# Optimization experiments

Hardware: AMD Instinct MI355X
Metric: run time of the kernel (lower is better)

Reference implementation:

```python
import jax, jax.numpy as jnp
import numpy as np

EPS = 1e-5

def _bn_relu(y, mean, var, scale, bias):
    # y: (b, c, n); eval-mode batchnorm over channel axis, then ReLU
    inv = scale / jnp.sqrt(var + EPS)
    return jax.nn.relu((y - mean[None, :, None]) * inv[None, :, None] + bias[None, :, None])

def setup_inputs() -> dict:
    key = jax.random.key(0)
    ks = jax.random.split(key, 6)
    b, c, n, cr = 4, 256, 4096, 32
    inp = {
        'x': jax.random.normal(ks[0], (b, c, n), jnp.float32),
        'w_q': jax.random.normal(ks[1], (cr, c), jnp.float32) * (1.0 / np.sqrt(c)),
        'w_k': jax.random.normal(ks[2], (cr, c), jnp.float32) * (1.0 / np.sqrt(c)),
        'w_v': jax.random.normal(ks[3], (c, c), jnp.float32) * (1.0 / np.sqrt(c)),
        'bn1_scale': jnp.ones((cr,), jnp.float32), 'bn1_bias': jnp.zeros((cr,), jnp.float32),
        'bn1_mean': jnp.zeros((cr,), jnp.float32), 'bn1_var': jnp.ones((cr,), jnp.float32),
        'bn2_scale': jnp.ones((cr,), jnp.float32), 'bn2_bias': jnp.zeros((cr,), jnp.float32),
        'bn2_mean': jnp.zeros((cr,), jnp.float32), 'bn2_var': jnp.ones((cr,), jnp.float32),
        'bn3_scale': jnp.ones((c,), jnp.float32), 'bn3_bias': jnp.zeros((c,), jnp.float32),
        'bn3_mean': jnp.zeros((c,), jnp.float32), 'bn3_var': jnp.ones((c,), jnp.float32),
        'gamma': jax.random.normal(ks[4], (1,), jnp.float32),
    }
    return inp

def reference(x, w_q, w_k, w_v,
              bn1_scale, bn1_bias, bn1_mean, bn1_var,
              bn2_scale, bn2_bias, bn2_mean, bn2_var,
              bn3_scale, bn3_bias, bn3_mean, bn3_var,
              gamma):
    # x: (b, c, n). Original views as (b, c, n, 1) so width=1, height=n.
    b, c, n = x.shape
    # 1x1 conv == channel matmul, then BN+ReLU
    q = _bn_relu(jnp.einsum('oc,bcn->bon', w_q, x), bn1_mean, bn1_var, bn1_scale, bn1_bias)  # (b, c', n)
    k = _bn_relu(jnp.einsum('oc,bcn->bon', w_k, x), bn2_mean, bn2_var, bn2_scale, bn2_bias)  # (b, c', n)
    v = _bn_relu(jnp.einsum('oc,bcn->bon', w_v, x), bn3_mean, bn3_var, bn3_scale, bn3_bias)  # (b, c, n)
    # energy_H: (b, n, n) with -inf diagonal (self-attention along 'height')
    energy_h = jnp.einsum('bdi,bdj->bij', q, k)
    eye = jnp.eye(n, dtype=bool)
    energy_h = jnp.where(eye[None], -jnp.inf, energy_h)
    # energy_W: width=1 -> per-position self energy (b, n)
    energy_w = jnp.sum(q * k, axis=1)
    # softmax over concat of n H-logits and 1 W-logit
    att = jax.nn.softmax(jnp.concatenate([energy_h, energy_w[..., None]], axis=-1), axis=-1)  # (b, n, n+1)
    att_h = att[..., :n]        # (b, n, n), query i -> key j
    att_w = att[..., n]         # (b, n)
    out_h = jnp.einsum('bcj,bij->bci', v, att_h)   # aggregate values along height
    out_w = v * att_w[:, None, :]                  # width=1 self term
    out = gamma[0] * (out_h + out_w) + x
    return out
```

## Files before the change

kernel.cpp:

```cpp
#include <hip/hip_runtime.h>

#define Bb 4
#define Cc 256
#define Nn 4096
#define CR 32
#define EPS_BN 1e-5f
#define SHIFT2 28.853900817779268f
#define LOG2E  1.4426950408889634f
#define JSPLIT 2
#define JSL (Nn / JSPLIT)
#define TJ 128
#define NTILES (JSL / TJ)

typedef __attribute__((ext_vector_type(8))) short short8;
typedef __attribute__((ext_vector_type(4))) float f32x4;

__device__ inline unsigned int pk2(float a, float b) {
    __bf16 ha = (__bf16)a, hb = (__bf16)b;
    unsigned short ra = __builtin_bit_cast(unsigned short, ha);
    unsigned short rb = __builtin_bit_cast(unsigned short, hb);
    return ((unsigned int)rb << 16) | ra;
}
__device__ inline float blo(unsigned int u) { return __uint_as_float(u << 16); }
__device__ inline float bhi(unsigned int u) { return __uint_as_float(u & 0xffff0000u); }
__device__ inline float ex2(float x) { return __builtin_amdgcn_exp2f(x); }

__global__ __launch_bounds__(256) void prep_w(
    const float* __restrict__ wq, const float* __restrict__ wk,
    const float* __restrict__ wv, __bf16* __restrict__ Wf)
{
    const int r16 = blockIdx.x;
    const int tid = threadIdx.x;
#pragma unroll
    for (int ss = 0; ss < 2; ++ss) {
        int s = tid + ss * 256;
        int kc = s >> 6, lane = s & 63;
        int R = r16 * 16 + (lane & 15);
        const float* src = (R < 32) ? (wq + (size_t)R * Cc)
                         : (R < 64) ? (wk + (size_t)(R - 32) * Cc)
                                    : (wv + (size_t)(R - 64) * Cc);
        const float* p = src + kc * 32 + (lane >> 4) * 8;
        float4 a = *(const float4*)p;
        float4 c2 = *(const float4*)(p + 4);
        uint4 pk = { pk2(a.x,a.y), pk2(a.z,a.w), pk2(c2.x,c2.y), pk2(c2.z,c2.w) };
        *(uint4*)&Wf[(((size_t)r16 * 8 + kc) * 64 + lane) * 8] = pk;
    }
}

__global__ __launch_bounds__(256) void split_x(
    const float* __restrict__ x,
    __bf16* __restrict__ xhi, __bf16* __restrict__ xlo)
{
    __shared__ __align__(16) float tile[64][68];
    const int tid = threadIdx.x;
    const int n0 = blockIdx.x * 64, c0 = blockIdx.y * 64, b = blockIdx.z;

    {
        int r = tid >> 2, q = tid & 3;
        const float* src = &x[(size_t)(b * Cc + c0 + r) * Nn + n0 + q * 16];
#pragma unroll
        for (int u = 0; u < 4; ++u)
            *(float4*)&tile[r][q * 16 + u * 4] = *(const float4*)&src[u * 4];
    }
    __syncthreads();

    {
        int nr = tid >> 2, oc = tid & 3;
        uint4 H[2], L[2];
#pragma unroll
        for (int u = 0; u < 2; ++u) {
            float h[8], lo8[8];
#pragma unroll
            for (int j = 0; j < 8; ++j) {
                float v = tile[oc * 16 + u * 8 + j][nr];
                float hh = (float)(__bf16)v;
                h[j] = hh; lo8[j] = v - hh;
            }
            H[u] = (uint4){ pk2(h[0],h[1]), pk2(h[2],h[3]), pk2(h[4],h[5]), pk2(h[6],h[7]) };
            L[u] = (uint4){ pk2(lo8[0],lo8[1]), pk2(lo8[2],lo8[3]), pk2(lo8[4],lo8[5]), pk2(lo8[6],lo8[7]) };
        }
        size_t base = (size_t)(b * Nn + n0 + nr) * Cc + c0 + oc * 16;
        *(uint4*)&xhi[base]     = H[0];
        *(uint4*)&xhi[base + 8] = H[1];
        *(uint4*)&xlo[base]     = L[0];
        *(uint4*)&xlo[base + 8] = L[1];
    }
}

__global__ __launch_bounds__(256) void qkv_kernel(
    const __bf16* __restrict__ xhi, const __bf16* __restrict__ xlo,
    const __bf16* __restrict__ Wf,
    const float* __restrict__ bn1s, const float* __restrict__ bn1b, const float* __restrict__ bn1m, const float* __restrict__ bn1v,
    const float* __restrict__ bn2s, const float* __restrict__ bn2b, const float* __restrict__ bn2m, const float* __restrict__ bn2v,
    const float* __restrict__ bn3s, const float* __restrict__ bn3b, const float* __restrict__ bn3m, const float* __restrict__ bn3v,
    __bf16* __restrict__ Qt, __bf16* __restrict__ Kt, __bf16* __restrict__ Vb)
{
    __shared__ __align__(16) __bf16 oT[128 * 136];

    const int tid = threadIdx.x;
    const int n0 = blockIdx.x * 128, g = blockIdx.y, b = blockIdx.z;
    const int lane = tid & 63, w = tid >> 6;
    const int l15 = lane & 15, l4 = lane >> 4;
    const int nmt = (g == 0) ? 4 : 8;
    const int r16b = (g == 0) ? 0 : 4 + (g - 1) * 8;

    const size_t bfoff = (size_t)(b * Nn + n0 + w * 32 + l15) * Cc + l4 * 8;
    const __bf16* bh0 = xhi + bfoff;
    const __bf16* bl0 = xlo + bfoff;

    f32x4 acc[8][2];
#pragma unroll
    for (int mt = 0; mt < 8; ++mt)
#pragma unroll
        for (int nt = 0; nt < 2; ++nt) acc[mt][nt] = (f32x4){0.f, 0.f, 0.f, 0.f};

    for (int kc = 0; kc < 8; ++kc) {
        short8 bh[2], bl[2];
#pragma unroll
        for (int nt = 0; nt < 2; ++nt) {
            bh[nt] = *(const short8*)&bh0[(size_t)(nt * 16) * Cc + kc * 32];
            bl[nt] = *(const short8*)&bl0[(size_t)(nt * 16) * Cc + kc * 32];
        }
#pragma unroll
        for (int mt = 0; mt < 8; ++mt) {
            if (mt < nmt) {
                short8 af = *(const short8*)&Wf[(((size_t)(r16b + mt) * 8 + kc) * 64 + lane) * 8];
#pragma unroll
                for (int nt = 0; nt < 2; ++nt) {
                    acc[mt][nt] = __builtin_amdgcn_mfma_f32_16x16x32_bf16(af, bh[nt], acc[mt][nt], 0, 0, 0);
                    acc[mt][nt] = __builtin_amdgcn_mfma_f32_16x16x32_bf16(af, bl[nt], acc[mt][nt], 0, 0, 0);
                }
            }
        }
    }

    if (g == 0) {
#pragma unroll
        for (int mt = 0; mt < 4; ++mt) {
            float scl[4], off[4];
#pragma unroll
            for (int r = 0; r < 4; ++r) {
                int R = mt * 16 + l4 * 4 + r;
                float s, o;
                if (R < 32) {
                    s = bn1s[R] * __frsqrt_rn(bn1v[R] + EPS_BN);
                    o = bn1b[R] - bn1m[R] * s;
                } else {
                    int row = R - 32;
                    s = bn2s[row] * __frsqrt_rn(bn2v[row] + EPS_BN);
                    o = bn2b[row] - bn2m[row] * s;
                    s *= LOG2E; o *= LOG2E;
                }
                scl[r] = s; off[r] = o;
            }
            __bf16* dst = (mt < 2) ? Qt : Kt;
            int d0 = (mt & 1) * 16 + l4 * 4;
#pragma unroll
            for (int nt = 0; nt < 2; ++nt) {
                f32x4 a = acc[mt][nt];
                float e0 = fmaxf(fmaf(a.x, scl[0], off[0]), 0.f);
                float e1 = fmaxf(fmaf(a.y, scl[1], off[1]), 0.f);
                float e2 = fmaxf(fmaf(a.z, scl[2], off[2]), 0.f);
                float e3 = fmaxf(fmaf(a.w, scl[3], off[3]), 0.f);
                uint2 p = { pk2(e0, e1), pk2(e2, e3) };
                int n = n0 + w * 32 + nt * 16 + l15;
                *(uint2*)&dst[(size_t)(b * Nn + n) * CR + d0] = p;
            }
        }
    } else {
        const int vr0 = (g - 1) * 128;
#pragma unroll
        for (int mt = 0; mt < 8; ++mt) {
            float scl[4], off[4];
#pragma unroll
            for (int r = 0; r < 4; ++r) {
                int row = vr0 + mt * 16 + l4 * 4 + r;
                float s = bn3s[row] * __frsqrt_rn(bn3v[row] + EPS_BN);
                scl[r] = s; off[r] = bn3b[row] - bn3m[row] * s;
            }
#pragma unroll
            for (int nt = 0; nt < 2; ++nt) {
                f32x4 a = acc[mt][nt];
                float e[4];
                e[0] = fmaxf(fmaf(a.x, scl[0], off[0]), 0.f);
                e[1] = fmaxf(fmaf(a.y, scl[1], off[1]), 0.f);
                e[2] = fmaxf(fmaf(a.z, scl[2], off[2]), 0.f);
                e[3] = fmaxf(fmaf(a.w, scl[3], off[3]), 0.f);
                int ncol = w * 32 + nt * 16 + l15;
#pragma unroll
                for (int r = 0; r < 4; ++r)
                    oT[(mt * 16 + l4 * 4 + r) * 136 + ncol] = (__bf16)e[r];
            }
        }
        __syncthreads();
        int rr = tid >> 1, qq = tid & 1;
        size_t vrow = (size_t)(b * Cc + vr0 + rr) * Nn + n0 + qq * 64;
#pragma unroll
        for (int e8 = 0; e8 < 8; ++e8)
            *(uint4*)&Vb[vrow + e8 * 8] = *(const uint4*)&oT[rr * 136 + qq * 64 + e8 * 8];
    }
}

__global__ __launch_bounds__(512) void attn_kernel(
    const __bf16* __restrict__ Qt, const __bf16* __restrict__ Kt,
    const __bf16* __restrict__ Vb,
    __bf16* __restrict__ PO, float* __restrict__ PL)
{
    __shared__ __align__(16) __bf16 sQ[64 * 40];
    __shared__ __align__(16) __bf16 sP[64 * 128];
    __shared__ __align__(16) float  sL[8][64];

    const int tid = threadIdx.x, lane = tid & 63, w = tid >> 6;
    const int b = blockIdx.z, js = blockIdx.y, iblk = blockIdx.x;
    const int i0 = iblk * 64;
    const int l15 = lane & 15, l4 = lane >> 4;

    if (tid < 256) {
        int i = tid >> 2, o = tid & 3;
        *(uint4*)&sQ[i * 40 + o * 8] =
            *(const uint4*)&Qt[(size_t)(b * Nn + i0 + i) * CR + o * 8];
    }
    __syncthreads();

    short8 qf[4];
#pragma unroll
    for (int it = 0; it < 4; ++it)
        qf[it] = *(const short8*)&sQ[(it * 16 + l15) * 40 + l4 * 8];

    f32x4 oacc[8];
#pragma unroll
    for (int z = 0; z < 8; ++z) oacc[z] = (f32x4){0.f, 0.f, 0.f, 0.f};
    float lp[4] = {0.f, 0.f, 0.f, 0.f};

    const size_t jb = (size_t)js * JSL;
    short8 kf = *(const short8*)&Kt[(size_t)(b * Nn + jb + 16 * w + l15) * CR + l4 * 8];
    const __bf16* vrow0 = Vb + (size_t)(b * Cc + w * 32 + l15) * Nn;

    char* sPb = (char*)sP;
    const int wcolw = w * 32 + l4 * 8;

    for (int t = 0; t < NTILES; ++t) {
        const size_t j0 = jb + (size_t)t * TJ;

        short8 v0[2], v1[2];
#pragma unroll
        for (int ct = 0; ct < 2; ++ct)
            v0[ct] = *(const short8*)&vrow0[(size_t)(ct * 16) * Nn + j0 + l4 * 8];
#pragma unroll
        for (int ct = 0; ct < 2; ++ct)
            v1[ct] = *(const short8*)&vrow0[(size_t)(ct * 16) * Nn + j0 + 32 + l4 * 8];

#pragma unroll
        for (int it = 0; it < 4; ++it) {
            f32x4 c0 = (f32x4){0.f, 0.f, 0.f, 0.f};
            c0 = __builtin_amdgcn_mfma_f32_16x16x32_bf16(kf, qf[it], c0, 0, 0, 0);
            float e0 = ex2(c0.x - SHIFT2);
            float e1 = ex2(c0.y - SHIFT2);
            float e2 = ex2(c0.z - SHIFT2);
            float e3 = ex2(c0.w - SHIFT2);
            lp[it] += (e0 + e1) + (e2 + e3);
            uint2 p2 = { pk2(e0, e1), pk2(e2, e3) };
            int row = it * 16 + l15;
            *(uint2*)(sPb + row * 256 + (wcolw ^ ((row & 7) << 4))) = p2;
        }
        __syncthreads();

        if (t + 1 < NTILES)
            kf = *(const short8*)&Kt[(size_t)(b * Nn + j0 + TJ + 16 * w + l15) * CR + l4 * 8];

        __builtin_amdgcn_s_setprio(1);
        {
            short8 pf[4];
#pragma unroll
            for (int it = 0; it < 4; ++it) {
                int row = it * 16 + l15;
                pf[it] = *(const short8*)(sPb + row * 256 + ((l4 * 16) ^ ((row & 7) << 4)));
            }
#pragma unroll
            for (int ct = 0; ct < 2; ++ct)
#pragma unroll
                for (int it = 0; it < 4; ++it)
                    oacc[it * 2 + ct] = __builtin_amdgcn_mfma_f32_16x16x32_bf16(
                        pf[it], v0[ct], oacc[it * 2 + ct], 0, 0, 0);
        }
#pragma unroll
        for (int ct = 0; ct < 2; ++ct)
            v0[ct] = *(const short8*)&vrow0[(size_t)(ct * 16) * Nn + j0 + 64 + l4 * 8];
        {
            short8 pf[4];
#pragma unroll
            for (int it = 0; it < 4; ++it) {
                int row = it * 16 + l15;
                pf[it] = *(const short8*)(sPb + row * 256 + ((64 + l4 * 16) ^ ((row & 7) << 4)));
            }
#pragma unroll
            for (int ct = 0; ct < 2; ++ct)
#pragma unroll
                for (int it = 0; it < 4; ++it)
                    oacc[it * 2 + ct] = __builtin_amdgcn_mfma_f32_16x16x32_bf16(
                        pf[it], v1[ct], oacc[it * 2 + ct], 0, 0, 0);
        }
#pragma unroll
        for (int ct = 0; ct < 2; ++ct)
            v1[ct] = *(const short8*)&vrow0[(size_t)(ct * 16) * Nn + j0 + 96 + l4 * 8];
        {
            short8 pf[4];
#pragma unroll
            for (int it = 0; it < 4; ++it) {
                int row = it * 16 + l15;
                pf[it] = *(const short8*)(sPb + row * 256 + ((128 + l4 * 16) ^ ((row & 7) << 4)));
            }
#pragma unroll
            for (int ct = 0; ct < 2; ++ct)
#pragma unroll
                for (int it = 0; it < 4; ++it)
                    oacc[it * 2 + ct] = __builtin_amdgcn_mfma_f32_16x16x32_bf16(
                        pf[it], v0[ct], oacc[it * 2 + ct], 0, 0, 0);
        }
        {
            short8 pf[4];
#pragma unroll
            for (int it = 0; it < 4; ++it) {
                int row = it * 16 + l15;
                pf[it] = *(const short8*)(sPb + row * 256 + ((192 + l4 * 16) ^ ((row & 7) << 4)));
            }
#pragma unroll
            for (int ct = 0; ct < 2; ++ct)
#pragma unroll
                for (int it = 0; it < 4; ++it)
                    oacc[it * 2 + ct] = __builtin_amdgcn_mfma_f32_16x16x32_bf16(
                        pf[it], v1[ct], oacc[it * 2 + ct], 0, 0, 0);
        }
        __builtin_amdgcn_s_setprio(0);
        __syncthreads();
    }

#pragma unroll
    for (int it = 0; it < 4; ++it) {
        float v = lp[it];
        v += __shfl_xor(v, 16);
        v += __shfl_xor(v, 32);
        if (lane < 16) sL[w][it * 16 + lane] = v;
    }
    __syncthreads();
    if (tid < 64) {
        float s = 0.f;
#pragma unroll
        for (int w8 = 0; w8 < 8; ++w8) s += sL[w8][tid];
        PL[(size_t)(js * Bb + b) * Nn + i0 + tid] = s;
    }

    const size_t base = (size_t)((js * Bb + b) * (Nn / 64) + iblk) * 16384;
#pragma unroll
    for (int it = 0; it < 4; ++it)
#pragma unroll
        for (int ct = 0; ct < 2; ++ct) {
            f32x4 a = oacc[it * 2 + ct];
            uint2 p = { pk2(a.x, a.y), pk2(a.z, a.w) };
            int g16 = w * 2 + ct;
            int s = (g16 >> 2) * 16 + it * 4 + (g16 & 3);
            *(uint2*)&PO[base + (size_t)(s * 64 + lane) * 4] = p;
        }
}

__global__ __launch_bounds__(256) void reduce_kernel(
    const __bf16* __restrict__ PO, const float* __restrict__ PL,
    const float* __restrict__ x, const float* __restrict__ gamma,
    float* __restrict__ out)
{
    __shared__ __align__(16) float oT[64 * 68];
    __shared__ float sLinv[64];

    const int tid = threadIdx.x;
    const int iblk = blockIdx.x, wq = blockIdx.y, b = blockIdx.z;
    const int i0 = iblk * 64;
    const int lane = tid & 63, ct = tid >> 6, l15 = lane & 15, l4 = lane >> 4;

    if (tid < 64) {
        float l = 0.f;
#pragma unroll
        for (int js = 0; js < JSPLIT; ++js)
            l += PL[(size_t)(js * Bb + b) * Nn + i0 + tid];
        sLinv[tid] = 1.0f / l;
    }

    float o[4][4];
#pragma unroll
    for (int it = 0; it < 4; ++it) {
        o[it][0] = o[it][1] = o[it][2] = o[it][3] = 0.f;
#pragma unroll
        for (int js = 0; js < JSPLIT; ++js) {
            size_t base = (size_t)((js * Bb + b) * (Nn / 64) + iblk) * 16384;
            uint2 v = *(const uint2*)&PO[base + (size_t)((((wq * 4 + it) * 4 + ct) * 64 + lane)) * 4];
            o[it][0] += blo(v.x); o[it][1] += bhi(v.x);
            o[it][2] += blo(v.y); o[it][3] += bhi(v.y);
        }
    }

    const int cl = ct * 16 + l15;
#pragma unroll
    for (int it = 0; it < 4; ++it) {
        float4 t4 = { o[it][0], o[it][1], o[it][2], o[it][3] };
        *(float4*)&oT[cl * 68 + it * 16 + l4 * 4] = t4;
    }
    __syncthreads();

    const float g = gamma[0];
    const int c_l = tid >> 2, icol = (tid & 3) * 16;
    const int cg = wq * 64 + c_l;
    const size_t gb = (size_t)(b * Cc + cg) * Nn + i0 + icol;
#pragma unroll
    for (int k4 = 0; k4 < 4; ++k4) {
        float4 ov = *(const float4*)&oT[c_l * 68 + icol + k4 * 4];
        float4 li = *(const float4*)&sLinv[icol + k4 * 4];
        float4 xv = *(const float4*)&x[gb + k4 * 4];
        float4 res;
        res.x = fmaf(g, ov.x * li.x, xv.x);
        res.y = fmaf(g, ov.y * li.y, xv.y);
        res.z = fmaf(g, ov.z * li.z, xv.z);
        res.w = fmaf(g, ov.w * li.w, xv.w);
        *(float4*)&out[gb + k4 * 4] = res;
    }
}

extern "C" void kernel_launch(void* const* d_in, const int* in_sizes, int n_in,
                              void* d_out, int out_size, void* d_ws, size_t ws_size,
                              hipStream_t stream)
{
    const float* x    = (const float*)d_in[0];
    const float* wq   = (const float*)d_in[1];
    const float* wk   = (const float*)d_in[2];
    const float* wv   = (const float*)d_in[3];
    const float* bn1s = (const float*)d_in[4];
    const float* bn1b = (const float*)d_in[5];
    const float* bn1m = (const float*)d_in[6];
    const float* bn1v = (const float*)d_in[7];
    const float* bn2s = (const float*)d_in[8];
    const float* bn2b = (const float*)d_in[9];
    const float* bn2m = (const float*)d_in[10];
    const float* bn2v = (const float*)d_in[11];
    const float* bn3s = (const float*)d_in[12];
    const float* bn3b = (const float*)d_in[13];
    const float* bn3m = (const float*)d_in[14];
    const float* bn3v = (const float*)d_in[15];
    const float* gmm  = (const float*)d_in[16];
    float* out = (float*)d_out;

    char* ws = (char*)d_ws;
    __bf16* Qt  = (__bf16*)(ws);
    __bf16* Kt  = (__bf16*)(ws + (1u << 20));
    __bf16* Vb  = (__bf16*)(ws + (2u << 20));
    __bf16* PO  = (__bf16*)(ws + (10u << 20));
    float*  PL  = (float*)(ws + (26u << 20));
    __bf16* Wf  = (__bf16*)(ws + (26u << 20) + 262144);
    __bf16* xhi = (__bf16*)(ws + (27u << 20));
    __bf16* xlo = (__bf16*)(ws + (35u << 20));

    prep_w<<<dim3(20), 256, 0, stream>>>(wq, wk, wv, Wf);

    split_x<<<dim3(Nn / 64, Cc / 64, Bb), 256, 0, stream>>>(x, xhi, xlo);

    qkv_kernel<<<dim3(Nn / 128, 3, Bb), 256, 0, stream>>>(
        xhi, xlo, Wf,
        bn1s, bn1b, bn1m, bn1v,
        bn2s, bn2b, bn2m, bn2v,
        bn3s, bn3b, bn3m, bn3v,
        Qt, Kt, Vb);

    attn_kernel<<<dim3(Nn / 64, JSPLIT, Bb), 512, 0, stream>>>(Qt, Kt, Vb, PO, PL);

    reduce_kernel<<<dim3(Nn / 64, 4, Bb), 256, 0, stream>>>(PO, PL, x, gmm, out);
}
```

Baseline: 203.0 us.

## Halve attention block to 4 waves, each covering 64 channels and 32 keys

The attention kernel now runs with 256 threads (4 waves) instead of 512. Each wave computes two 16-key score tiles per 128-key tile and accumulates 64 value channels (16 accumulators instead of 8). This doubles per-wave work and register reuse of the P fragments, and halves the redundant P loads from LDS across waves. In exchange each wave holds more registers, which may lower occupancy, and the PO output layout is remapped to match.

```diff
diff --git a/kernel.cpp b/kernel.cpp
--- a/kernel.cpp
+++ b/kernel.cpp
@@ -201,21 +201,21 @@
     }
 }
 
-__global__ __launch_bounds__(512) void attn_kernel(
+__global__ __launch_bounds__(256) void attn_kernel(
     const __bf16* __restrict__ Qt, const __bf16* __restrict__ Kt,
     const __bf16* __restrict__ Vb,
     __bf16* __restrict__ PO, float* __restrict__ PL)
 {
     __shared__ __align__(16) __bf16 sQ[64 * 40];
     __shared__ __align__(16) __bf16 sP[64 * 128];
-    __shared__ __align__(16) float  sL[8][64];
+    __shared__ __align__(16) float  sL[4][64];
 
     const int tid = threadIdx.x, lane = tid & 63, w = tid >> 6;
     const int b = blockIdx.z, js = blockIdx.y, iblk = blockIdx.x;
     const int i0 = iblk * 64;
     const int l15 = lane & 15, l4 = lane >> 4;
 
-    if (tid < 256) {
+    {
         int i = tid >> 2, o = tid & 3;
         *(uint4*)&sQ[i * 40 + o * 8] =
             *(const uint4*)&Qt[(size_t)(b * Nn + i0 + i) * CR + o * 8];
@@ -227,46 +227,55 @@
     for (int it = 0; it < 4; ++it)
         qf[it] = *(const short8*)&sQ[(it * 16 + l15) * 40 + l4 * 8];
 
-    f32x4 oacc[8];
-#pragma unroll
-    for (int z = 0; z < 8; ++z) oacc[z] = (f32x4){0.f, 0.f, 0.f, 0.f};
+    f32x4 oacc[16];
+#pragma unroll
+    for (int z = 0; z < 16; ++z) oacc[z] = (f32x4){0.f, 0.f, 0.f, 0.f};
     float lp[4] = {0.f, 0.f, 0.f, 0.f};
 
     const size_t jb = (size_t)js * JSL;
-    short8 kf = *(const short8*)&Kt[(size_t)(b * Nn + jb + 16 * w + l15) * CR + l4 * 8];
-    const __bf16* vrow0 = Vb + (size_t)(b * Cc + w * 32 + l15) * Nn;
+    short8 kf[2];
+#pragma unroll
+    for (int s = 0; s < 2; ++s)
+        kf[s] = *(const short8*)&Kt[(size_t)(b * Nn + jb + w * 32 + s * 16 + l15) * CR + l4 * 8];
+    const __bf16* vrow0 = Vb + (size_t)(b * Cc + w * 64 + l15) * Nn;
 
     char* sPb = (char*)sP;
-    const int wcolw = w * 32 + l4 * 8;
+    const int wcolw = w * 64 + l4 * 8;
 
     for (int t = 0; t < NTILES; ++t) {
         const size_t j0 = jb + (size_t)t * TJ;
 
-        short8 v0[2], v1[2];
-#pragma unroll
-        for (int ct = 0; ct < 2; ++ct)
+        short8 v0[4], v1[4];
+#pragma unroll
+        for (int ct = 0; ct < 4; ++ct)
             v0[ct] = *(const short8*)&vrow0[(size_t)(ct * 16) * Nn + j0 + l4 * 8];
 #pragma unroll
-        for (int ct = 0; ct < 2; ++ct)
+        for (int ct = 0; ct < 4; ++ct)
             v1[ct] = *(const short8*)&vrow0[(size_t)(ct * 16) * Nn + j0 + 32 + l4 * 8];
 
 #pragma unroll
-        for (int it = 0; it < 4; ++it) {
-            f32x4 c0 = (f32x4){0.f, 0.f, 0.f, 0.f};
-            c0 = __builtin_amdgcn_mfma_f32_16x16x32_bf16(kf, qf[it], c0, 0, 0, 0);
-            float e0 = ex2(c0.x - SHIFT2);
-            float e1 = ex2(c0.y - SHIFT2);
-            float e2 = ex2(c0.z - SHIFT2);
-            float e3 = ex2(c0.w - SHIFT2);
-            lp[it] += (e0 + e1) + (e2 + e3);
-            uint2 p2 = { pk2(e0, e1), pk2(e2, e3) };
-            int row = it * 16 + l15;
-            *(uint2*)(sPb + row * 256 + (wcolw ^ ((row & 7) << 4))) = p2;
+        for (int s = 0; s < 2; ++s) {
+#pragma unroll
+            for (int it = 0; it < 4; ++it) {
+                f32x4 c0 = (f32x4){0.f, 0.f, 0.f, 0.f};
+                c0 = __builtin_amdgcn_mfma_f32_16x16x32_bf16(kf[s], qf[it], c0, 0, 0, 0);
+                float e0 = ex2(c0.x - SHIFT2);
+                float e1 = ex2(c0.y - SHIFT2);
+                float e2 = ex2(c0.z - SHIFT2);
+                float e3 = ex2(c0.w - SHIFT2);
+                lp[it] += (e0 + e1) + (e2 + e3);
+                uint2 p2 = { pk2(e0, e1), pk2(e2, e3) };
+                int row = it * 16 + l15;
+                *(uint2*)(sPb + row * 256 + ((wcolw + s * 32) ^ ((row & 7) << 4))) = p2;
+            }
         }
         __syncthreads();
 
-        if (t + 1 < NTILES)
-            kf = *(const short8*)&Kt[(size_t)(b * Nn + j0 + TJ + 16 * w + l15) * CR + l4 * 8];
+        if (t + 1 < NTILES) {
+#pragma unroll
+            for (int s = 0; s < 2; ++s)
+                kf[s] = *(const short8*)&Kt[(size_t)(b * Nn + j0 + TJ + w * 32 + s * 16 + l15) * CR + l4 * 8];
+        }
 
         __builtin_amdgcn_s_setprio(1);
         {
@@ -277,14 +286,14 @@
                 pf[it] = *(const short8*)(sPb + row * 256 + ((l4 * 16) ^ ((row & 7) << 4)));
             }
 #pragma unroll
-            for (int ct = 0; ct < 2; ++ct)
+            for (int ct = 0; ct < 4; ++ct)
 #pragma unroll
                 for (int it = 0; it < 4; ++it)
-                    oacc[it * 2 + ct] = __builtin_amdgcn_mfma_f32_16x16x32_bf16(
-                        pf[it], v0[ct], oacc[it * 2 + ct], 0, 0, 0);
-        }
-#pragma unroll
-        for (int ct = 0; ct < 2; ++ct)
+                    oacc[it * 4 + ct] = __builtin_amdgcn_mfma_f32_16x16x32_bf16(
+                        pf[it], v0[ct], oacc[it * 4 + ct], 0, 0, 0);
+        }
+#pragma unroll
+        for (int ct = 0; ct < 4; ++ct)
             v0[ct] = *(const short8*)&vrow0[(size_t)(ct * 16) * Nn + j0 + 64 + l4 * 8];
         {
             short8 pf[4];
@@ -294,14 +303,14 @@
                 pf[it] = *(const short8*)(sPb + row * 256 + ((64 + l4 * 16) ^ ((row & 7) << 4)));
             }
 #pragma unroll
-            for (int ct = 0; ct < 2; ++ct)
+            for (int ct = 0; ct < 4; ++ct)
 #pragma unroll
                 for (int it = 0; it < 4; ++it)
-                    oacc[it * 2 + ct] = __builtin_amdgcn_mfma_f32_16x16x32_bf16(
-                        pf[it], v1[ct], oacc[it * 2 + ct], 0, 0, 0);
-        }
-#pragma unroll
-        for (int ct = 0; ct < 2; ++ct)
+                    oacc[it * 4 + ct] = __builtin_amdgcn_mfma_f32_16x16x32_bf16(
+                        pf[it], v1[ct], oacc[it * 4 + ct], 0, 0, 0);
+        }
+#pragma unroll
+        for (int ct = 0; ct < 4; ++ct)
             v1[ct] = *(const short8*)&vrow0[(size_t)(ct * 16) * Nn + j0 + 96 + l4 * 8];
         {
             short8 pf[4];
@@ -311,11 +320,11 @@
                 pf[it] = *(const short8*)(sPb + row * 256 + ((128 + l4 * 16) ^ ((row & 7) << 4)));
             }
 #pragma unroll
-            for (int ct = 0; ct < 2; ++ct)
+            for (int ct = 0; ct < 4; ++ct)
 #pragma unroll
                 for (int it = 0; it < 4; ++it)
-                    oacc[it * 2 + ct] = __builtin_amdgcn_mfma_f32_16x16x32_bf16(
-                        pf[it], v0[ct], oacc[it * 2 + ct], 0, 0, 0);
+                    oacc[it * 4 + ct] = __builtin_amdgcn_mfma_f32_16x16x32_bf16(
+                        pf[it], v0[ct], oacc[it * 4 + ct], 0, 0, 0);
         }
         {
             short8 pf[4];
@@ -325,11 +334,11 @@
                 pf[it] = *(const short8*)(sPb + row * 256 + ((192 + l4 * 16) ^ ((row & 7) << 4)));
             }
 #pragma unroll
-            for (int ct = 0; ct < 2; ++ct)
+            for (int ct = 0; ct < 4; ++ct)
 #pragma unroll
                 for (int it = 0; it < 4; ++it)
-                    oacc[it * 2 + ct] = __builtin_amdgcn_mfma_f32_16x16x32_bf16(
-                        pf[it], v1[ct], oacc[it * 2 + ct], 0, 0, 0);
+                    oacc[it * 4 + ct] = __builtin_amdgcn_mfma_f32_16x16x32_bf16(
+                        pf[it], v1[ct], oacc[it * 4 + ct], 0, 0, 0);
         }
         __builtin_amdgcn_s_setprio(0);
         __syncthreads();
@@ -343,23 +352,18 @@
         if (lane < 16) sL[w][it * 16 + lane] = v;
     }
     __syncthreads();
-    if (tid < 64) {
-        float s = 0.f;
-#pragma unroll
-        for (int w8 = 0; w8 < 8; ++w8) s += sL[w8][tid];
-        PL[(size_t)(js * Bb + b) * Nn + i0 + tid] = s;
-    }
+    if (tid < 64)
+        PL[(size_t)(js * Bb + b) * Nn + i0 + tid] =
+            sL[0][tid] + sL[1][tid] + sL[2][tid] + sL[3][tid];
 
     const size_t base = (size_t)((js * Bb + b) * (Nn / 64) + iblk) * 16384;
 #pragma unroll
     for (int it = 0; it < 4; ++it)
 #pragma unroll
-        for (int ct = 0; ct < 2; ++ct) {
-            f32x4 a = oacc[it * 2 + ct];
+        for (int ct = 0; ct < 4; ++ct) {
+            f32x4 a = oacc[it * 4 + ct];
             uint2 p = { pk2(a.x, a.y), pk2(a.z, a.w) };
-            int g16 = w * 2 + ct;
-            int s = (g16 >> 2) * 16 + it * 4 + (g16 & 3);
-            *(uint2*)&PO[base + (size_t)(s * 64 + lane) * 4] = p;
+            *(uint2*)&PO[base + (size_t)((((w * 4 + it) * 4 + ct) * 64 + lane)) * 4] = p;
         }
 }
 
@@ -467,7 +471,7 @@
         bn3s, bn3b, bn3m, bn3v,
         Qt, Kt, Vb);
 
-    attn_kernel<<<dim3(Nn / 64, JSPLIT, Bb), 512, 0, stream>>>(Qt, Kt, Vb, PO, PL);
+    attn_kernel<<<dim3(Nn / 64, JSPLIT, Bb), 256, 0, stream>>>(Qt, Kt, Vb, PO, PL);
 
     reduce_kernel<<<dim3(Nn / 64, 4, Bb), 256, 0, stream>>>(PO, PL, x, gmm, out);
 }
```

Result: slower. 208.6 us (+2.8%).
